# Kernel optimization log

Hardware: AMD Instinct MI355X
Metric: run time of the kernel (lower is better)

The kernel has to match this reference:

```python
import jax, jax.numpy as jnp
import numpy as np

E, N, D, OUT = 1_600_000, 50_000, 128, 128
EPS_STD = 1e-5
EPS_BN = 1e-5


def setup_inputs() -> dict:
    key = jax.random.key(0)
    k0, k1, k2, k3 = jax.random.split(key, 4)
    inputs = jax.random.normal(k0, (E, D), dtype=jnp.float32)
    index = jax.random.randint(k1, (E,), 0, N, dtype=jnp.int32)
    # learned params
    deg_emb = jax.random.normal(k2, (100, D), dtype=jnp.float32) * 0.02  # nn.Embedding(100, nin)
    W = jax.random.normal(k3, (5 * D, OUT), dtype=jnp.float32) / np.sqrt(5 * D)  # bias-free Linear
    gamma = jnp.ones((OUT,), jnp.float32)   # BatchNorm1d weight
    beta = jnp.zeros((OUT,), jnp.float32)   # BatchNorm1d bias
    return {"inputs": inputs, "index": index, "deg_emb": deg_emb,
            "W": W, "gamma": gamma, "beta": beta, "dim_size": N}


def _aggregate(inputs, index, deg_emb, dim_size):
    ones = jnp.ones((inputs.shape[0],), inputs.dtype)
    cnt = jax.ops.segment_sum(ones, index, num_segments=dim_size)          # [N]
    safe = jnp.maximum(cnt, 1.0)[:, None]                                   # torch_scatter mean clamps count>=1
    s = jax.ops.segment_sum(inputs, index, num_segments=dim_size)          # [N, D]
    sq = jax.ops.segment_sum(inputs * inputs, index, num_segments=dim_size)
    mean = s / safe
    mean_sq = sq / safe
    mn = jax.ops.segment_min(inputs, index, num_segments=dim_size)
    mx = jax.ops.segment_max(inputs, index, num_segments=dim_size)
    has = (cnt > 0)[:, None]
    mn = jnp.where(has, mn, 0.0)  # empty segments -> 0 like torch_scatter
    mx = jnp.where(has, mx, 0.0)
    std = jnp.sqrt(jax.nn.relu(mean_sq - mean * mean) + EPS_STD)
    deg = jnp.minimum(cnt.astype(jnp.int32), 99)  # degree embedding lookup (table size 100)
    return jnp.concatenate([mean, mn, mx, std, deg_emb[deg]], axis=-1)     # [N, 5D]


def reference(inputs, index, deg_emb, W, gamma, beta, dim_size):
    x = _aggregate(inputs, index, deg_emb, dim_size)
    h = x @ W                                      # Linear, no bias
    mu = h.mean(axis=0)
    var = h.var(axis=0)                            # biased, as BatchNorm training mode
    h = (h - mu) / jnp.sqrt(var + EPS_BN) * gamma + beta
    return jax.nn.relu(h)
```

## Files before the change

### kernel.cpp

```cpp
#include <hip/hip_runtime.h>
#include <cstdint>
#include <cstddef>

#define NNODES 50000
#define DIM 128
#define K5 640
#define OUTD 128
#define MPAD 50048
#define EPS_STD 1e-5f
#define EPS_BN 1e-5f
#define LDA 40
#define LDB 40

typedef __attribute__((ext_vector_type(8))) __bf16 bf16x8;
typedef __attribute__((ext_vector_type(4))) float f32x4;

__device__ __forceinline__ unsigned short f2bf(float f) {
  unsigned int u = __float_as_uint(f);
  u = u + 0x7fffu + ((u >> 16) & 1u);
  return (unsigned short)(u >> 16);
}

__global__ void hist_k(const int* __restrict__ idx, int* __restrict__ counts, int E) {
  int e = blockIdx.x * 256 + threadIdx.x;
  if (e < E) atomicAdd(&counts[idx[e]], 1);
}

__global__ void scan1_k(const int* __restrict__ counts, int* __restrict__ offsets,
                        int* __restrict__ blocksums, int n) {
  __shared__ int sh[256];
  int t = threadIdx.x;
  int i = blockIdx.x * 256 + t;
  int v = (i < n) ? counts[i] : 0;
  sh[t] = v; __syncthreads();
  for (int off = 1; off < 256; off <<= 1) {
    int add = (t >= off) ? sh[t - off] : 0;
    __syncthreads();
    sh[t] += add;
    __syncthreads();
  }
  if (i < n) offsets[i] = sh[t] - v;
  if (t == 255) blocksums[blockIdx.x] = sh[t];
}

__global__ void scan2_k(int* __restrict__ blocksums, int nb) {
  __shared__ int sh[256];
  int t = threadIdx.x;
  int v = (t < nb) ? blocksums[t] : 0;
  sh[t] = v; __syncthreads();
  for (int off = 1; off < 256; off <<= 1) {
    int add = (t >= off) ? sh[t - off] : 0;
    __syncthreads();
    sh[t] += add;
    __syncthreads();
  }
  if (t < nb) blocksums[t] = sh[t] - v;
}

__global__ void scan3_k(int* __restrict__ offsets, const int* __restrict__ blocksums,
                        int* __restrict__ cursor, int n) {
  int i = blockIdx.x * 256 + threadIdx.x;
  if (i < n) {
    int o = offsets[i] + blocksums[blockIdx.x];
    offsets[i] = o;
    cursor[i] = o;
  }
}

__global__ void scatter_k(const int* __restrict__ idx, int* __restrict__ cursor,
                          int* __restrict__ sorted, int E) {
  int e = blockIdx.x * 256 + threadIdx.x;
  if (e < E) {
    int p = atomicAdd(&cursor[idx[e]], 1);
    sorted[p] = e;
  }
}

__global__ void convW_k(const float* __restrict__ W, unsigned short* __restrict__ Wt) {
  int t = blockIdx.x * 256 + threadIdx.x;
  if (t >= OUTD * K5) return;
  int c = t / K5, k = t % K5;
  Wt[t] = f2bf(W[(size_t)k * OUTD + c]);
}

__global__ __launch_bounds__(256) void agg_k(
    const float* __restrict__ inp, const int* __restrict__ sorted,
    const int* __restrict__ offsets, const int* __restrict__ counts,
    const float* __restrict__ deg_emb, unsigned short* __restrict__ x) {
  const int wid  = threadIdx.x >> 6;
  const int node = blockIdx.x * 4 + wid;
  const int lane = threadIdx.x & 63;
  const int half = lane >> 5;
  const int sl   = lane & 31;
  const int c0   = sl * 4;
  unsigned short* xrow = x + (size_t)node * K5;

  if (node >= NNODES) {
    if (half == 0) {
      ushort4 z = {0, 0, 0, 0};
      #pragma unroll
      for (int sgm = 0; sgm < 5; sgm++) *(ushort4*)(xrow + sgm * DIM + c0) = z;
    }
    return;
  }

  const int start = offsets[node];
  const int cnt   = counts[node];
  float s[4] = {0.f, 0.f, 0.f, 0.f}, q[4] = {0.f, 0.f, 0.f, 0.f};
  float mn[4], mx[4];
  #pragma unroll
  for (int i = 0; i < 4; i++) { mn[i] = INFINITY; mx[i] = -INFINITY; }

  for (int j0 = 0; j0 < cnt; j0 += 64) {
    const int lim = min(64, cnt - j0);
    int myid = 0;
    if (j0 + lane < cnt) myid = sorted[start + j0 + lane];
    for (int j = 0; j < lim; j += 2) {
      const int r = j + half;
      const int e = __shfl(myid, r);
      if (r < lim) {
        const float4 v4 = *(const float4*)(inp + (size_t)e * DIM + c0);
        const float v[4] = {v4.x, v4.y, v4.z, v4.w};
        #pragma unroll
        for (int i = 0; i < 4; i++) {
          s[i] += v[i];
          q[i] += v[i] * v[i];
          mn[i] = fminf(mn[i], v[i]);
          mx[i] = fmaxf(mx[i], v[i]);
        }
      }
    }
  }
  #pragma unroll
  for (int i = 0; i < 4; i++) {
    s[i] += __shfl_xor(s[i], 32);
    q[i] += __shfl_xor(q[i], 32);
    mn[i] = fminf(mn[i], __shfl_xor(mn[i], 32));
    mx[i] = fmaxf(mx[i], __shfl_xor(mx[i], 32));
  }
  if (half) return;

  const float inv = 1.0f / (float)max(cnt, 1);
  const int deg = min(cnt, 99);
  const float4 e4 = *(const float4*)(deg_emb + (size_t)deg * DIM + c0);
  const float emb[4] = {e4.x, e4.y, e4.z, e4.w};
  float mean[4], sd[4];
  #pragma unroll
  for (int i = 0; i < 4; i++) {
    mean[i] = s[i] * inv;
    float var = q[i] * inv - mean[i] * mean[i];
    sd[i] = sqrtf(fmaxf(var, 0.f) + EPS_STD);
    if (cnt == 0) { mn[i] = 0.f; mx[i] = 0.f; }
  }
  { ushort4 u = {f2bf(mean[0]), f2bf(mean[1]), f2bf(mean[2]), f2bf(mean[3])};
    *(ushort4*)(xrow + 0 * DIM + c0) = u; }
  { ushort4 u = {f2bf(mn[0]), f2bf(mn[1]), f2bf(mn[2]), f2bf(mn[3])};
    *(ushort4*)(xrow + 1 * DIM + c0) = u; }
  { ushort4 u = {f2bf(mx[0]), f2bf(mx[1]), f2bf(mx[2]), f2bf(mx[3])};
    *(ushort4*)(xrow + 2 * DIM + c0) = u; }
  { ushort4 u = {f2bf(sd[0]), f2bf(sd[1]), f2bf(sd[2]), f2bf(sd[3])};
    *(ushort4*)(xrow + 3 * DIM + c0) = u; }
  { ushort4 u = {f2bf(emb[0]), f2bf(emb[1]), f2bf(emb[2]), f2bf(emb[3])};
    *(ushort4*)(xrow + 4 * DIM + c0) = u; }
}

__global__ __launch_bounds__(256) void gemm_k(const unsigned short* __restrict__ x,
                                              const unsigned short* __restrict__ Wt,
                                              float* __restrict__ h) {
  __shared__ unsigned short As[64 * LDA];
  __shared__ unsigned short Bs[128 * LDB];
  const int t = threadIdx.x;
  const int m0 = blockIdx.x * 64;
  const int w = t >> 6, lane = t & 63;
  const int lm = lane & 15, lq = lane >> 4;

  f32x4 acc[8];
  #pragma unroll
  for (int i = 0; i < 8; i++) acc[i] = (f32x4){0.f, 0.f, 0.f, 0.f};

  const int arow = t >> 2, akoff = (t & 3) * 8;
  const int bt0 = t * 8, bt1 = 2048 + t * 8;
  const int bc0 = bt0 >> 5, bk0 = bt0 & 31;
  const int bc1 = bt1 >> 5, bk1 = bt1 & 31;

  for (int k0 = 0; k0 < K5; k0 += 32) {
    *(uint4*)&As[arow * LDA + akoff] = *(const uint4*)&x[(size_t)(m0 + arow) * K5 + k0 + akoff];
    *(uint4*)&Bs[bc0 * LDB + bk0]    = *(const uint4*)&Wt[(size_t)bc0 * K5 + k0 + bk0];
    *(uint4*)&Bs[bc1 * LDB + bk1]    = *(const uint4*)&Wt[(size_t)bc1 * K5 + k0 + bk1];
    __syncthreads();
    const bf16x8 a = *(const bf16x8*)&As[(w * 16 + lm) * LDA + lq * 8];
    #pragma unroll
    for (int tt = 0; tt < 8; tt++) {
      const bf16x8 b = *(const bf16x8*)&Bs[(tt * 16 + lm) * LDB + lq * 8];
      acc[tt] = __builtin_amdgcn_mfma_f32_16x16x32_bf16(a, b, acc[tt], 0, 0, 0);
    }
    __syncthreads();
  }
  #pragma unroll
  for (int tt = 0; tt < 8; tt++) {
    #pragma unroll
    for (int r = 0; r < 4; r++) {
      const int row = m0 + w * 16 + lq * 4 + r;
      if (row < NNODES) h[(size_t)row * OUTD + tt * 16 + lm] = acc[tt][r];
    }
  }
}

__global__ void stats_k(const float* __restrict__ h, float* __restrict__ colsum,
                        float* __restrict__ colsumsq) {
  const int t = threadIdx.x;
  const int col = t & 127;
  const int rh = t >> 7;
  const int rend = min(blockIdx.x * 128 + 128, NNODES);
  float s = 0.f, q = 0.f;
  for (int r = blockIdx.x * 128 + rh; r < rend; r += 2) {
    const float v = h[(size_t)r * OUTD + col];
    s += v; q += v * v;
  }
  atomicAdd(&colsum[col], s);
  atomicAdd(&colsumsq[col], q);
}

__global__ void norm_k(float* __restrict__ h, const float* __restrict__ colsum,
                       const float* __restrict__ colsumsq, const float* __restrict__ gamma,
                       const float* __restrict__ beta) {
  const int i = blockIdx.x * 256 + threadIdx.x;
  const int total = NNODES * OUTD / 4;
  if (i >= total) return;
  const int c0 = (i * 4) & (OUTD - 1);
  const float invN = 1.0f / (float)NNODES;
  float4 v = *(const float4*)(h + (size_t)i * 4);
  float out[4] = {v.x, v.y, v.z, v.w};
  #pragma unroll
  for (int j = 0; j < 4; j++) {
    const int c = c0 + j;
    const float mu = colsum[c] * invN;
    const float var = colsumsq[c] * invN - mu * mu;
    const float rs = rsqrtf(var + EPS_BN);
    const float tv = (out[j] - mu) * rs * gamma[c] + beta[c];
    out[j] = fmaxf(tv, 0.f);
  }
  float4 o4 = {out[0], out[1], out[2], out[3]};
  *(float4*)(h + (size_t)i * 4) = o4;
}

extern "C" void kernel_launch(void* const* d_in, const int* in_sizes, int n_in,
                              void* d_out, int out_size, void* d_ws, size_t ws_size,
                              hipStream_t stream) {
  const float* inputs  = (const float*)d_in[0];
  const int*   index   = (const int*)d_in[1];
  const float* deg_emb = (const float*)d_in[2];
  const float* W       = (const float*)d_in[3];
  const float* gamma   = (const float*)d_in[4];
  const float* beta    = (const float*)d_in[5];
  const int E = in_sizes[1];

  char* ws = (char*)d_ws;
  size_t o = 0;
  int* counts = (int*)(ws + o);       o += (size_t)NNODES * 4;
  float* colsum = (float*)(ws + o);   o += 128 * 4;
  float* colsumsq = (float*)(ws + o); o += 128 * 4;
  const size_t zero_bytes = o;
  o = (o + 255) & ~(size_t)255;
  int* offsets = (int*)(ws + o);      o += (size_t)NNODES * 4;
  o = (o + 255) & ~(size_t)255;
  int* cursor = (int*)(ws + o);       o += (size_t)NNODES * 4;
  o = (o + 255) & ~(size_t)255;
  int* blocksums = (int*)(ws + o);    o += 256 * 4;
  o = (o + 255) & ~(size_t)255;
  int* sorted = (int*)(ws + o);       o += (size_t)E * 4;
  o = (o + 255) & ~(size_t)255;
  unsigned short* Wt = (unsigned short*)(ws + o); o += (size_t)OUTD * K5 * 2;
  o = (o + 255) & ~(size_t)255;
  unsigned short* x = (unsigned short*)(ws + o);  o += (size_t)MPAD * K5 * 2;

  float* h = (float*)d_out;

  hipMemsetAsync(counts, 0, zero_bytes, stream);
  hist_k<<<(E + 255) / 256, 256, 0, stream>>>(index, counts, E);
  const int NB = (NNODES + 255) / 256;
  scan1_k<<<NB, 256, 0, stream>>>(counts, offsets, blocksums, NNODES);
  scan2_k<<<1, 256, 0, stream>>>(blocksums, NB);
  scan3_k<<<NB, 256, 0, stream>>>(offsets, blocksums, cursor, NNODES);
  scatter_k<<<(E + 255) / 256, 256, 0, stream>>>(index, cursor, sorted, E);
  convW_k<<<(OUTD * K5 + 255) / 256, 256, 0, stream>>>(W, Wt);
  agg_k<<<MPAD / 4, 256, 0, stream>>>(inputs, sorted, offsets, counts, deg_emb, x);
  gemm_k<<<MPAD / 64, 256, 0, stream>>>(x, Wt, h);
  stats_k<<<(NNODES + 127) / 128, 256, 0, stream>>>(h, colsum, colsumsq);
  norm_k<<<(NNODES * OUTD / 4 + 255) / 256, 256, 0, stream>>>(h, colsum, colsumsq, gamma, beta);
}
```

Before: 1.359 ms.

## Unroll gather loop in aggregation and fuse column stats into GEMM epilogue

The aggregation kernel's edge loop is unrolled to issue four independent row gathers per half-wave before reducing, which raises memory-level parallelism on the random-access input reads. Separately, the BatchNorm column sum and sum-of-squares are now computed in the GEMM epilogue through wave shuffles and a shared-memory reduction, with one atomic per column per block. This removes the separate stats kernel and its re-read of h. In exchange the GEMM uses more registers and shared memory, and the floating-point summation order changes.

```diff
diff --git a/kernel.cpp b/kernel.cpp
--- a/kernel.cpp
+++ b/kernel.cpp
@@ -115,12 +115,34 @@
     const int lim = min(64, cnt - j0);
     int myid = 0;
     if (j0 + lane < cnt) myid = sorted[start + j0 + lane];
-    for (int j = 0; j < lim; j += 2) {
+    int j = 0;
+    for (; j + 8 <= lim; j += 8) {
+      const int e0 = __shfl(myid, j + 0 + half);
+      const int e1 = __shfl(myid, j + 2 + half);
+      const int e2 = __shfl(myid, j + 4 + half);
+      const int e3 = __shfl(myid, j + 6 + half);
+      const float4 a0 = *(const float4*)(inp + (size_t)e0 * DIM + c0);
+      const float4 a1 = *(const float4*)(inp + (size_t)e1 * DIM + c0);
+      const float4 a2 = *(const float4*)(inp + (size_t)e2 * DIM + c0);
+      const float4 a3 = *(const float4*)(inp + (size_t)e3 * DIM + c0);
+      const float v0[4] = {a0.x, a0.y, a0.z, a0.w};
+      const float v1[4] = {a1.x, a1.y, a1.z, a1.w};
+      const float v2[4] = {a2.x, a2.y, a2.z, a2.w};
+      const float v3[4] = {a3.x, a3.y, a3.z, a3.w};
+      #pragma unroll
+      for (int i = 0; i < 4; i++) {
+        s[i] += v0[i] + v1[i] + v2[i] + v3[i];
+        q[i] += v0[i] * v0[i] + v1[i] * v1[i] + v2[i] * v2[i] + v3[i] * v3[i];
+        mn[i] = fminf(fminf(fminf(mn[i], v0[i]), fminf(v1[i], v2[i])), v3[i]);
+        mx[i] = fmaxf(fmaxf(fmaxf(mx[i], v0[i]), fmaxf(v1[i], v2[i])), v3[i]);
+      }
+    }
+    for (; j < lim; j += 2) {
       const int r = j + half;
-      const int e = __shfl(myid, r);
+      const int e = __shfl(myid, r < lim ? r : (lim - 1));
       if (r < lim) {
-        const float4 v4 = *(const float4*)(inp + (size_t)e * DIM + c0);
-        const float v[4] = {v4.x, v4.y, v4.z, v4.w};
+        const float4 a = *(const float4*)(inp + (size_t)e * DIM + c0);
+        const float v[4] = {a.x, a.y, a.z, a.w};
         #pragma unroll
         for (int i = 0; i < 4; i++) {
           s[i] += v[i];
@@ -166,9 +188,13 @@
 
 __global__ __launch_bounds__(256) void gemm_k(const unsigned short* __restrict__ x,
                                               const unsigned short* __restrict__ Wt,
-                                              float* __restrict__ h) {
+                                              float* __restrict__ h,
+                                              float* __restrict__ colsum,
+                                              float* __restrict__ colsumsq) {
   __shared__ unsigned short As[64 * LDA];
   __shared__ unsigned short Bs[128 * LDB];
+  __shared__ float sh_s[4 * 128];
+  __shared__ float sh_q[4 * 128];
   const int t = threadIdx.x;
   const int m0 = blockIdx.x * 64;
   const int w = t >> 6, lane = t & 63;
@@ -196,29 +222,42 @@
     }
     __syncthreads();
   }
+  float psum[8], psq[8];
   #pragma unroll
   for (int tt = 0; tt < 8; tt++) {
+    psum[tt] = 0.f; psq[tt] = 0.f;
     #pragma unroll
     for (int r = 0; r < 4; r++) {
       const int row = m0 + w * 16 + lq * 4 + r;
-      if (row < NNODES) h[(size_t)row * OUTD + tt * 16 + lm] = acc[tt][r];
-    }
-  }
-}
-
-__global__ void stats_k(const float* __restrict__ h, float* __restrict__ colsum,
-                        float* __restrict__ colsumsq) {
-  const int t = threadIdx.x;
-  const int col = t & 127;
-  const int rh = t >> 7;
-  const int rend = min(blockIdx.x * 128 + 128, NNODES);
-  float s = 0.f, q = 0.f;
-  for (int r = blockIdx.x * 128 + rh; r < rend; r += 2) {
-    const float v = h[(size_t)r * OUTD + col];
-    s += v; q += v * v;
-  }
-  atomicAdd(&colsum[col], s);
-  atomicAdd(&colsumsq[col], q);
+      if (row < NNODES) {
+        const float v = acc[tt][r];
+        h[(size_t)row * OUTD + tt * 16 + lm] = v;
+        psum[tt] += v;
+        psq[tt]  += v * v;
+      }
+    }
+  }
+  #pragma unroll
+  for (int tt = 0; tt < 8; tt++) {
+    psum[tt] += __shfl_xor(psum[tt], 16);
+    psum[tt] += __shfl_xor(psum[tt], 32);
+    psq[tt]  += __shfl_xor(psq[tt], 16);
+    psq[tt]  += __shfl_xor(psq[tt], 32);
+  }
+  if (lq == 0) {
+    #pragma unroll
+    for (int tt = 0; tt < 8; tt++) {
+      sh_s[w * 128 + tt * 16 + lm] = psum[tt];
+      sh_q[w * 128 + tt * 16 + lm] = psq[tt];
+    }
+  }
+  __syncthreads();
+  if (t < 128) {
+    float s = sh_s[t] + sh_s[128 + t] + sh_s[256 + t] + sh_s[384 + t];
+    float qv = sh_q[t] + sh_q[128 + t] + sh_q[256 + t] + sh_q[384 + t];
+    atomicAdd(&colsum[t], s);
+    atomicAdd(&colsumsq[t], qv);
+  }
 }
 
 __global__ void norm_k(float* __restrict__ h, const float* __restrict__ colsum,
@@ -285,7 +324,6 @@
   scatter_k<<<(E + 255) / 256, 256, 0, stream>>>(index, cursor, sorted, E);
   convW_k<<<(OUTD * K5 + 255) / 256, 256, 0, stream>>>(W, Wt);
   agg_k<<<MPAD / 4, 256, 0, stream>>>(inputs, sorted, offsets, counts, deg_emb, x);
-  gemm_k<<<MPAD / 64, 256, 0, stream>>>(x, Wt, h);
-  stats_k<<<(NNODES + 127) / 128, 256, 0, stream>>>(h, colsum, colsumsq);
+  gemm_k<<<MPAD / 64, 256, 0, stream>>>(x, Wt, h, colsum, colsumsq);
   norm_k<<<(NNODES * OUTD / 4 + 255) / 256, 256, 0, stream>>>(h, colsum, colsumsq, gamma, beta);
 }
```

New measurement: 1.319 ms. 1.03x faster.
